# Optimization experiments

Measured on AMD Instinct MI355X. Metric: run time of the kernel, lower is better.

The kernel has to match this reference:

```python
import jax, jax.numpy as jnp
import numpy as np

B, N_RES, N_ATOM, C_S, C_OUT = 2, 2048, 16384, 384, 50


def setup_inputs() -> dict:
    key = jax.random.key(0)
    k1, k2, k3 = jax.random.split(key, 3)
    # [B, n_res, c_s] single embedding
    s = jax.random.normal(k1, (B, N_RES, C_S), dtype=jnp.float32)
    # one-hot token->atom map: each atom selects exactly one residue
    atom_to_res = jax.random.randint(k2, (B, N_ATOM), 0, N_RES)
    token_to_atom_idx = jax.nn.one_hot(atom_to_res, N_RES, dtype=jnp.float32)  # [B, n_atom, n_res]
    # Linear(c_s, c_out) params (torch convention: W [c_out, c_s], b [c_out])
    W = jax.random.normal(k3, (C_OUT, C_S), dtype=jnp.float32) * 0.02
    b = jnp.zeros((C_OUT,), dtype=jnp.float32)
    return {"s": s, "token_to_atom_idx": token_to_atom_idx, "W": W, "b": b}


def reference(s, token_to_atom_idx, W, b):
    # sum_r one_hot[b,a,r] * s[b,r,c] -> broadcast-sum (a gather in disguise)
    atom_s = jnp.einsum('bar,brc->bac', token_to_atom_idx, s)  # [B, n_atom, c_s]
    logits = jnp.einsum('bac,oc->bao', atom_s, W) + b          # [B, n_atom, c_out]
    return logits
```

## Files before the change

kernel.cpp:

```cpp
#include <hip/hip_runtime.h>

#define B 2
#define N_RES 2048
#define N_ATOM 16384
#define C_S 384
#define C_OUT 50

#define SCAN_BLOCKS 8192
#define PROJ_BLOCKS 1024

typedef float nfloat4 __attribute__((ext_vector_type(4)));

__global__ __launch_bounds__(256) void fused_scan_proj(const float* __restrict__ s,
                                                       const float* __restrict__ W,
                                                       const float* __restrict__ bias,
                                                       const float* __restrict__ onehot,
                                                       float* __restrict__ proj,
                                                       int* __restrict__ idx) {
    __shared__ float srow[4][C_S];
    int wave = threadIdx.x >> 6;
    int lane = threadIdx.x & 63;

    if (blockIdx.x < SCAN_BLOCKS) {
        int a = (blockIdx.x << 2) + wave;
        const float* row = onehot + (size_t)a * N_RES;
        int r = 0;
        #pragma unroll 1
        for (int iter = 0; iter < N_RES / 256; ++iter) {
            int base = iter * 256 + (lane << 2);
            nfloat4 v = __builtin_nontemporal_load((const nfloat4*)(row + base));
            int j = -1;
            if (v.x != 0.f) j = 0;
            else if (v.y != 0.f) j = 1;
            else if (v.z != 0.f) j = 2;
            else if (v.w != 0.f) j = 3;
            unsigned long long mask = __ballot(j >= 0);
            if (mask) {
                int src = (int)__ffsll(mask) - 1;
                r = __shfl(base + j, src);
                break;
            }
        }
        if (lane == 0) idx[a] = r;
    } else {
        int rr = ((blockIdx.x - SCAN_BLOCKS) << 2) + wave;
        const float4* sp = (const float4*)(s + (size_t)rr * C_S);
        float4* srp = (float4*)srow[wave];
        for (int i = lane; i < C_S / 4; i += 64) srp[i] = sp[i];
        __syncthreads();
        if (lane < C_OUT) {
            const float* wp = W + lane * C_S;
            float acc = bias[lane];
            #pragma unroll 4
            for (int c = 0; c < C_S; c += 4) {
                float4 w4 = *(const float4*)(wp + c);
                acc += srow[wave][c]     * w4.x + srow[wave][c + 1] * w4.y
                     + srow[wave][c + 2] * w4.z + srow[wave][c + 3] * w4.w;
            }
            proj[(size_t)rr * C_OUT + lane] = acc;
        }
    }
}

__global__ __launch_bounds__(256) void gather_kernel(const int* __restrict__ idx,
                                                     const float* __restrict__ proj,
                                                     float* __restrict__ out) {
    int wave = threadIdx.x >> 6;
    int lane = threadIdx.x & 63;
    int a = (blockIdx.x << 2) + wave;
    int r = idx[a];
    int b = a >> 14;
    if (lane < C_OUT) {
        out[(size_t)a * C_OUT + lane] = proj[((size_t)b * N_RES + r) * C_OUT + lane];
    }
}

extern "C" void kernel_launch(void* const* d_in, const int* in_sizes, int n_in,
                              void* d_out, int out_size, void* d_ws, size_t ws_size,
                              hipStream_t stream) {
    const float* s      = (const float*)d_in[0];
    const float* onehot = (const float*)d_in[1];
    const float* W      = (const float*)d_in[2];
    const float* bias   = (const float*)d_in[3];
    float* out  = (float*)d_out;

    float* proj = (float*)d_ws;
    int*   idx  = (int*)((char*)d_ws + (1 << 20));

    fused_scan_proj<<<SCAN_BLOCKS + PROJ_BLOCKS, 256, 0, stream>>>(s, W, bias, onehot,
                                                                   proj, idx);
    gather_kernel<<<SCAN_BLOCKS, 256, 0, stream>>>(idx, proj, out);
}
```

Before: 381.0 us.

## Replace per-row early-exit one-hot scan with flat full-bandwidth streaming scan

The per-atom wave scan that walked each one-hot row serially until it found the nonzero is replaced. Instead, every thread streams eight independent float4 loads spread across the whole one-hot tensor and writes the row index wherever it finds a nonzero. This removes the serial, latency-bound loop with its early exit and keeps many loads in flight. The cost is reading the entire tensor instead of about half of it on average. Projection blocks now come first in the grid, and the gather launch size is expressed in terms of the problem dimensions.

After: 379.0 us. About the same (-0.5%).

```diff
diff --git a/kernel.cpp b/kernel.cpp
--- a/kernel.cpp
+++ b/kernel.cpp
@@ -6,8 +6,11 @@
 #define C_S 384
 #define C_OUT 50
 
+#define PROJ_BLOCKS 1024
 #define SCAN_BLOCKS 8192
-#define PROJ_BLOCKS 1024
+#define TOTAL_F4 (B * N_ATOM * N_RES / 4)
+#define SCAN_STRIDE (SCAN_BLOCKS * 256)
+#define SCAN_ITERS (TOTAL_F4 / SCAN_STRIDE)
 
 typedef float nfloat4 __attribute__((ext_vector_type(4)));
 
@@ -21,29 +24,25 @@
     int wave = threadIdx.x >> 6;
     int lane = threadIdx.x & 63;
 
-    if (blockIdx.x < SCAN_BLOCKS) {
-        int a = (blockIdx.x << 2) + wave;
-        const float* row = onehot + (size_t)a * N_RES;
-        int r = 0;
-        #pragma unroll 1
-        for (int iter = 0; iter < N_RES / 256; ++iter) {
-            int base = iter * 256 + (lane << 2);
-            nfloat4 v = __builtin_nontemporal_load((const nfloat4*)(row + base));
-            int j = -1;
-            if (v.x != 0.f) j = 0;
-            else if (v.y != 0.f) j = 1;
-            else if (v.z != 0.f) j = 2;
-            else if (v.w != 0.f) j = 3;
-            unsigned long long mask = __ballot(j >= 0);
-            if (mask) {
-                int src = (int)__ffsll(mask) - 1;
-                r = __shfl(base + j, src);
-                break;
+    if (blockIdx.x >= PROJ_BLOCKS) {
+        size_t t0 = (size_t)(blockIdx.x - PROJ_BLOCKS) * 256 + threadIdx.x;
+        nfloat4 v[SCAN_ITERS];
+        #pragma unroll
+        for (int k = 0; k < SCAN_ITERS; ++k)
+            v[k] = __builtin_nontemporal_load(
+                       (const nfloat4*)onehot + t0 + (size_t)k * SCAN_STRIDE);
+        #pragma unroll
+        for (int k = 0; k < SCAN_ITERS; ++k) {
+            nfloat4 x = v[k];
+            if (x.x != 0.f || x.y != 0.f || x.z != 0.f || x.w != 0.f) {
+                size_t e = (t0 + (size_t)k * SCAN_STRIDE) << 2;
+                int j = (x.x != 0.f) ? 0 : (x.y != 0.f) ? 1 : (x.z != 0.f) ? 2 : 3;
+                size_t ee = e + j;
+                idx[ee >> 11] = (int)(ee & (N_RES - 1));
             }
         }
-        if (lane == 0) idx[a] = r;
     } else {
-        int rr = ((blockIdx.x - SCAN_BLOCKS) << 2) + wave;
+        int rr = (blockIdx.x << 2) + wave;
         const float4* sp = (const float4*)(s + (size_t)rr * C_S);
         float4* srp = (float4*)srow[wave];
         for (int i = lane; i < C_S / 4; i += 64) srp[i] = sp[i];
@@ -87,7 +86,7 @@
     float* proj = (float*)d_ws;
     int*   idx  = (int*)((char*)d_ws + (1 << 20));
 
-    fused_scan_proj<<<SCAN_BLOCKS + PROJ_BLOCKS, 256, 0, stream>>>(s, W, bias, onehot,
+    fused_scan_proj<<<PROJ_BLOCKS + SCAN_BLOCKS, 256, 0, stream>>>(s, W, bias, onehot,
                                                                    proj, idx);
-    gather_kernel<<<SCAN_BLOCKS, 256, 0, stream>>>(idx, proj, out);
+    gather_kernel<<<(B * N_ATOM) / 4, 256, 0, stream>>>(idx, proj, out);
 }
```
